# Optimization experiments

Measured on AMD Instinct MI355X. Metric: run time of the kernel, lower is better.

## Reference

```python
import jax, jax.numpy as jnp
import numpy as np

HEADS = 8
DIM_HEAD = 64
QUERY_DIM = 512
INNER = HEADS * DIM_HEAD
T = 16
MAX_REL = 16  # == temporal_length
SCALE = DIM_HEAD ** -0.5


def _rel_idx(length_q, length_k):
    rq = jnp.arange(length_q)
    rk = jnp.arange(length_k)
    dist = rk[None, :] - rq[:, None]
    return jnp.clip(dist, -MAX_REL, MAX_REL) + MAX_REL  # [Tq, Tk] in [0, 2*MAX_REL]


def setup_inputs() -> dict:
    key = jax.random.key(0)
    ks = jax.random.split(key, 8)
    B = 2048
    s = 0.02
    return {
        "x": jax.random.normal(ks[0], (B, T, QUERY_DIM), dtype=jnp.float32),
        "Wq": jax.random.normal(ks[1], (QUERY_DIM, INNER), dtype=jnp.float32) * s,
        "Wk": jax.random.normal(ks[2], (QUERY_DIM, INNER), dtype=jnp.float32) * s,
        "Wv": jax.random.normal(ks[3], (QUERY_DIM, INNER), dtype=jnp.float32) * s,
        "Wo": jax.random.normal(ks[4], (INNER, QUERY_DIM), dtype=jnp.float32) * s,
        "bo": jnp.zeros((QUERY_DIM,), dtype=jnp.float32),
        "rel_k_table": jax.random.normal(ks[5], (2 * MAX_REL + 1, DIM_HEAD), dtype=jnp.float32) * s,
        "rel_v_table": jax.random.normal(ks[6], (2 * MAX_REL + 1, DIM_HEAD), dtype=jnp.float32) * s,
    }


def reference(x, Wq, Wk, Wv, Wo, bo, rel_k_table, rel_v_table):
    B, N, _ = x.shape
    # projections (Linear without bias)
    def split_heads(t):
        return t.reshape(B, N, HEADS, DIM_HEAD).transpose(0, 2, 1, 3)  # [B, H, N, D]
    q = split_heads(x @ Wq)
    k = split_heads(x @ Wk)
    v = split_heads(x @ Wv)

    sim = jnp.einsum('bhid,bhjd->bhij', q, k) * SCALE
    idx = _rel_idx(N, N)                     # [N, N]
    k2 = rel_k_table[idx]                    # [N, N, D]
    sim = sim + jnp.einsum('bhtd,tsd->bhts', q, k2) * SCALE

    attn = jax.nn.softmax(sim, axis=-1)
    out = jnp.einsum('bhij,bhjd->bhid', attn, v)
    v2 = rel_v_table[idx]                    # [N, N, D]
    out = out + jnp.einsum('bhts,tsd->bhtd', attn, v2)

    out = out.transpose(0, 2, 1, 3).reshape(B, N, INNER)
    return out @ Wo + bo
```

## Files before the change

### kernel.cpp

```cpp
#include <hip/hip_runtime.h>
#include <stdint.h>


using bf16x8 = __attribute__((ext_vector_type(8))) short;
using f32x4  = __attribute__((ext_vector_type(4))) float;

#define AS3P(p) ((__attribute__((address_space(3))) void*)(p))
#define AS1P(p) ((const __attribute__((address_space(1))) void*)(p))

__device__ __forceinline__ uint16_t f2bf(float f) {
  unsigned int x = __builtin_bit_cast(unsigned int, f);
  x += 0x7fffu + ((x >> 16) & 1u);
  return (uint16_t)(x >> 16);
}

__global__ void cast_kernel(const float* __restrict__ in, uint16_t* __restrict__ out, int n8) {
  int i = blockIdx.x * 256 + threadIdx.x;
  if (i >= n8) return;
  float4 a = ((const float4*)in)[i * 2];
  float4 b = ((const float4*)in)[i * 2 + 1];
  uint4 r;
  r.x = (uint32_t)f2bf(a.x) | ((uint32_t)f2bf(a.y) << 16);
  r.y = (uint32_t)f2bf(a.z) | ((uint32_t)f2bf(a.w) << 16);
  r.z = (uint32_t)f2bf(b.x) | ((uint32_t)f2bf(b.y) << 16);
  r.w = (uint32_t)f2bf(b.z) | ((uint32_t)f2bf(b.w) << 16);
  ((uint4*)out)[i] = r;
}

__global__ void transpose_cast4(const float* __restrict__ Wq, const float* __restrict__ Wk,
                                const float* __restrict__ Wv, const float* __restrict__ Wo,
                                uint16_t* __restrict__ WqkvT, uint16_t* __restrict__ WoT) {
  __shared__ float tile[32][33];
  const int z = blockIdx.z;
  const float* src = (z == 0) ? Wq : (z == 1) ? Wk : (z == 2) ? Wv : Wo;
  uint16_t* dst = (z == 3) ? WoT : (WqkvT + z * 262144);
  int tx = threadIdx.x, ty = threadIdx.y;
  int c0 = blockIdx.x * 32, r0 = blockIdx.y * 32;
  #pragma unroll
  for (int k = 0; k < 4; ++k)
    tile[ty + 8 * k][tx] = src[(r0 + ty + 8 * k) * 512 + c0 + tx];
  __syncthreads();
  #pragma unroll
  for (int k = 0; k < 4; ++k)
    dst[(c0 + ty + 8 * k) * 512 + r0 + tx] = f2bf(tile[tx][ty + 8 * k]);
}

template<int OUT_MODE, int KDIM>
__global__ __launch_bounds__(256, 2) void gemm256(
    const uint16_t* __restrict__ A, const uint16_t* __restrict__ B,
    void* __restrict__ C, const float* __restrict__ bias, int N, int nbx) {
  constexpr int NT = KDIM / 32;
  __shared__ __align__(16) uint16_t ldsA[3][8192];
  __shared__ __align__(16) uint16_t ldsB[3][4096];
  __shared__ __align__(16) uint16_t ldsO[4][1024];
  const int tid = threadIdx.x;
  const int w = tid >> 6, l = tid & 63;
  const int lr = l & 15, kc = l >> 4;
  const int wm = w >> 1, wn = w & 1;
  const int cpx = gridDim.x >> 3;
  const int id = blockIdx.x;
  const int swz = (id & 7) * cpx + (id >> 3);
  const int by = swz / nbx, bx = swz - by * nbx;
  const int mBase = by * 256, nBase = bx * 128;
  const int g8 = l >> 3;
  const int sub = (l & 7) ^ g8;
  const uint16_t* gA = A + (size_t)(mBase + w * 64 + g8 * 2 + (sub >> 2)) * KDIM + (sub & 3) * 8;
  const uint16_t* gB = B + (size_t)(nBase + w * 32 + g8 * 2 + (sub >> 2)) * KDIM + (sub & 3) * 8;
  int offA[8], offB[4];
  #pragma unroll
  for (int m = 0; m < 8; ++m) {
    int row = wm * 128 + m * 16 + lr;
    int rp = row >> 1, sb = ((row & 1) << 2) | kc;
    offA[m] = rp * 128 + ((sb ^ (rp & 7)) << 4);
  }
  #pragma unroll
  for (int n = 0; n < 4; ++n) {
    int row = wn * 64 + n * 16 + lr;
    int rp = row >> 1, sb = ((row & 1) << 2) | kc;
    offB[n] = rp * 128 + ((sb ^ (rp & 7)) << 4);
  }
  f32x4 acc[8][4] = {};

#define STAGE_A(t, bf) do { \
    uint16_t* d = &ldsA[bf][w * 2048]; \
    const uint16_t* s = gA + (t) * 32; \
    __builtin_amdgcn_global_load_lds(AS1P(s),              AS3P(d),        16, 0, 0); \
    __builtin_amdgcn_global_load_lds(AS1P(s + 16 * KDIM),  AS3P(d + 512),  16, 0, 0); \
    __builtin_amdgcn_global_load_lds(AS1P(s + 32 * KDIM),  AS3P(d + 1024), 16, 0, 0); \
    __builtin_amdgcn_global_load_lds(AS1P(s + 48 * KDIM),  AS3P(d + 1536), 16, 0, 0); \
  } while (0)
#define STAGE_B(t, bf) do { \
    uint16_t* d = &ldsB[bf][w * 1024]; \
    const uint16_t* s = gB + (t) * 32; \
    __builtin_amdgcn_global_load_lds(AS1P(s),              AS3P(d),        16, 0, 0); \
    __builtin_amdgcn_global_load_lds(AS1P(s + 16 * KDIM),  AS3P(d + 512),  16, 0, 0); \
  } while (0)

  STAGE_A(0, 0); STAGE_B(0, 0);
  STAGE_A(1, 1); STAGE_B(1, 1);
  asm volatile("s_waitcnt vmcnt(6)" ::: "memory");
  __builtin_amdgcn_s_barrier();

  #pragma unroll
  for (int t = 0; t < NT; ++t) {
    const int bi = t % 3;
    const int si = (t + 2) % 3;
    const char* bufA = (const char*)&ldsA[bi][0];
    const char* bufB = (const char*)&ldsB[bi][0];
    if (t + 2 < NT) STAGE_A(t + 2, si);
    if (t + 2 < NT) asm volatile("s_waitcnt vmcnt(4)" ::: "memory");
    else            asm volatile("s_waitcnt vmcnt(0)" ::: "memory");
    bf16x8 a0 = *(const bf16x8*)(bufA + offA[0]);
    bf16x8 a1 = *(const bf16x8*)(bufA + offA[1]);
    bf16x8 a2 = *(const bf16x8*)(bufA + offA[2]);
    bf16x8 a3 = *(const bf16x8*)(bufA + offA[3]);
    bf16x8 b0 = *(const bf16x8*)(bufB + offB[0]);
    bf16x8 b1 = *(const bf16x8*)(bufB + offB[1]);
    bf16x8 b2 = *(const bf16x8*)(bufB + offB[2]);
    bf16x8 b3 = *(const bf16x8*)(bufB + offB[3]);
    __builtin_amdgcn_sched_barrier(0);
    __builtin_amdgcn_s_barrier();
    asm volatile("s_waitcnt lgkmcnt(0)" ::: "memory");
    __builtin_amdgcn_sched_barrier(0);
    __builtin_amdgcn_s_setprio(1);
    acc[0][0] = __builtin_amdgcn_mfma_f32_16x16x32_bf16(a0, b0, acc[0][0], 0, 0, 0);
    acc[0][1] = __builtin_amdgcn_mfma_f32_16x16x32_bf16(a0, b1, acc[0][1], 0, 0, 0);
    acc[0][2] = __builtin_amdgcn_mfma_f32_16x16x32_bf16(a0, b2, acc[0][2], 0, 0, 0);
    acc[0][3] = __builtin_amdgcn_mfma_f32_16x16x32_bf16(a0, b3, acc[0][3], 0, 0, 0);
    acc[1][0] = __builtin_amdgcn_mfma_f32_16x16x32_bf16(a1, b0, acc[1][0], 0, 0, 0);
    acc[1][1] = __builtin_amdgcn_mfma_f32_16x16x32_bf16(a1, b1, acc[1][1], 0, 0, 0);
    acc[1][2] = __builtin_amdgcn_mfma_f32_16x16x32_bf16(a1, b2, acc[1][2], 0, 0, 0);
    acc[1][3] = __builtin_amdgcn_mfma_f32_16x16x32_bf16(a1, b3, acc[1][3], 0, 0, 0);
    acc[2][0] = __builtin_amdgcn_mfma_f32_16x16x32_bf16(a2, b0, acc[2][0], 0, 0, 0);
    acc[2][1] = __builtin_amdgcn_mfma_f32_16x16x32_bf16(a2, b1, acc[2][1], 0, 0, 0);
    acc[2][2] = __builtin_amdgcn_mfma_f32_16x16x32_bf16(a2, b2, acc[2][2], 0, 0, 0);
    acc[2][3] = __builtin_amdgcn_mfma_f32_16x16x32_bf16(a2, b3, acc[2][3], 0, 0, 0);
    acc[3][0] = __builtin_amdgcn_mfma_f32_16x16x32_bf16(a3, b0, acc[3][0], 0, 0, 0);
    acc[3][1] = __builtin_amdgcn_mfma_f32_16x16x32_bf16(a3, b1, acc[3][1], 0, 0, 0);
    acc[3][2] = __builtin_amdgcn_mfma_f32_16x16x32_bf16(a3, b2, acc[3][2], 0, 0, 0);
    acc[3][3] = __builtin_amdgcn_mfma_f32_16x16x32_bf16(a3, b3, acc[3][3], 0, 0, 0);
    __builtin_amdgcn_s_setprio(0);
    __builtin_amdgcn_sched_barrier(0);
    __builtin_amdgcn_s_barrier();
    if (t + 2 < NT) STAGE_B(t + 2, si);
    bf16x8 a4 = *(const bf16x8*)(bufA + offA[4]);
    bf16x8 a5 = *(const bf16x8*)(bufA + offA[5]);
    bf16x8 a6 = *(const bf16x8*)(bufA + offA[6]);
    bf16x8 a7 = *(const bf16x8*)(bufA + offA[7]);
    __builtin_amdgcn_sched_barrier(0);
    __builtin_amdgcn_s_barrier();
    asm volatile("s_waitcnt lgkmcnt(0)" ::: "memory");
    __builtin_amdgcn_sched_barrier(0);
    __builtin_amdgcn_s_setprio(1);
    acc[4][0] = __builtin_amdgcn_mfma_f32_16x16x32_bf16(a4, b0, acc[4][0], 0, 0, 0);
    acc[4][1] = __builtin_amdgcn_mfma_f32_16x16x32_bf16(a4, b1, acc[4][1], 0, 0, 0);
    acc[4][2] = __builtin_amdgcn_mfma_f32_16x16x32_bf16(a4, b2, acc[4][2], 0, 0, 0);
    acc[4][3] = __builtin_amdgcn_mfma_f32_16x16x32_bf16(a4, b3, acc[4][3], 0, 0, 0);
    acc[5][0] = __builtin_amdgcn_mfma_f32_16x16x32_bf16(a5, b0, acc[5][0], 0, 0, 0);
    acc[5][1] = __builtin_amdgcn_mfma_f32_16x16x32_bf16(a5, b1, acc[5][1], 0, 0, 0);
    acc[5][2] = __builtin_amdgcn_mfma_f32_16x16x32_bf16(a5, b2, acc[5][2], 0, 0, 0);
    acc[5][3] = __builtin_amdgcn_mfma_f32_16x16x32_bf16(a5, b3, acc[5][3], 0, 0, 0);
    acc[6][0] = __builtin_amdgcn_mfma_f32_16x16x32_bf16(a6, b0, acc[6][0], 0, 0, 0);
    acc[6][1] = __builtin_amdgcn_mfma_f32_16x16x32_bf16(a6, b1, acc[6][1], 0, 0, 0);
    acc[6][2] = __builtin_amdgcn_mfma_f32_16x16x32_bf16(a6, b2, acc[6][2], 0, 0, 0);
    acc[6][3] = __builtin_amdgcn_mfma_f32_16x16x32_bf16(a6, b3, acc[6][3], 0, 0, 0);
    acc[7][0] = __builtin_amdgcn_mfma_f32_16x16x32_bf16(a7, b0, acc[7][0], 0, 0, 0);
    acc[7][1] = __builtin_amdgcn_mfma_f32_16x16x32_bf16(a7, b1, acc[7][1], 0, 0, 0);
    acc[7][2] = __builtin_amdgcn_mfma_f32_16x16x32_bf16(a7, b2, acc[7][2], 0, 0, 0);
    acc[7][3] = __builtin_amdgcn_mfma_f32_16x16x32_bf16(a7, b3, acc[7][3], 0, 0, 0);
    __builtin_amdgcn_s_setprio(0);
    __builtin_amdgcn_sched_barrier(0);
    __builtin_amdgcn_s_barrier();
  }
#undef STAGE_A
#undef STAGE_B
  if (OUT_MODE == 1) {
    uint16_t* oW = &ldsO[w][0];
    const int t2 = l >> 3, c2 = l & 7;
    const int grp = bx * 2 + wn;
    const int z = grp >> 3, h = grp & 7;
    uint16_t* gO = (uint16_t*)C + (size_t)h * 6291456 +
                   (size_t)(mBase + wm * 128 + t2) * 192 + z * 64 + c2 * 8;
    #pragma unroll
    for (int m = 0; m < 8; ++m) {
      #pragma unroll
      for (int n = 0; n < 4; ++n)
        #pragma unroll
        for (int r = 0; r < 4; ++r) {
          const int tt = kc * 4 + r;
          const int d = n * 16 + lr;
          const int col = (((d >> 3) ^ (tt & 7)) << 3) | (d & 7);
          oW[tt * 64 + col] = f2bf(acc[m][n][r]);
        }
      asm volatile("s_waitcnt lgkmcnt(0)" ::: "memory");
      __builtin_amdgcn_sched_barrier(0);
      bf16x8 s0 = *(const bf16x8*)(oW + t2 * 64 + (((c2 ^ (t2 & 7)) << 3)));
      bf16x8 s1 = *(const bf16x8*)(oW + (8 + t2) * 64 + (((c2 ^ (t2 & 7)) << 3)));
      *(bf16x8*)(gO + (size_t)(m * 16) * 192) = s0;
      *(bf16x8*)(gO + (size_t)(m * 16 + 8) * 192) = s1;
      asm volatile("s_waitcnt lgkmcnt(0)" ::: "memory");
      __builtin_amdgcn_sched_barrier(0);
    }
  } else {
    #pragma unroll
    for (int m = 0; m < 8; ++m)
      #pragma unroll
      for (int n = 0; n < 4; ++n) {
        const int col = nBase + wn * 64 + n * 16 + lr;
        #pragma unroll
        for (int r = 0; r < 4; ++r) {
          const int row = mBase + wm * 128 + m * 16 + kc * 4 + r;
          ((float*)C)[(size_t)row * N + col] = acc[m][n][r] + bias[col];
        }
      }
  }
}

__global__ __launch_bounds__(512) void attn_kernel(
    const uint16_t* __restrict__ qkv,
    const float* __restrict__ relk, const float* __restrict__ relv,
    uint16_t* __restrict__ outA) {
  __shared__ __align__(16) uint16_t relkS[33 * 72];
  __shared__ __align__(16) uint16_t relvT[64 * 40];
  __shared__ __align__(16) uint16_t vT[8][64 * 24];
  __shared__ float attnS[8][16 * 17];
  const int tid = threadIdx.x;
  for (int e = tid; e < 33 * 64; e += 512) {
    int j = e >> 6, d = e & 63;
    relkS[j * 72 + d] = f2bf(relk[e]);
    relvT[d * 40 + j] = f2bf(relv[e]);
  }
  const int w = tid >> 6, l = tid & 63;
  const int bh = blockIdx.x * 8 + w;
  const int b = bh >> 3, h = bh & 7;
  const int lr = l & 15, kc = l >> 4;
  const uint16_t* base = qkv + (size_t)h * 6291456 + (size_t)(b * 16) * 192;
  const uint16_t* qrow = base + lr * 192;
  bf16x8 aq0 = *(const bf16x8*)(qrow + kc * 8);
  bf16x8 aq1 = *(const bf16x8*)(qrow + 32 + kc * 8);
  const uint16_t* krow = qrow + 64;
  bf16x8 bk0 = *(const bf16x8*)(krow + kc * 8);
  bf16x8 bk1 = *(const bf16x8*)(krow + 32 + kc * 8);
  {
    const int s = l >> 2, dg = l & 3;
    const uint16_t* vrow = base + s * 192 + 128 + dg * 16;
    uint4 v0 = *(const uint4*)vrow;
    uint4 v1 = *(const uint4*)(vrow + 8);
    uint16_t tmp[16];
    *(uint4*)(tmp) = v0; *(uint4*)(tmp + 8) = v1;
    #pragma unroll
    for (int i = 0; i < 16; ++i)
      vT[w][(dg * 16 + i) * 24 + s] = tmp[i];
  }
  __syncthreads();
  const f32x4 zero = {0.f, 0.f, 0.f, 0.f};
  f32x4 sim = __builtin_amdgcn_mfma_f32_16x16x32_bf16(aq0, bk0, zero, 0, 0, 0);
  sim = __builtin_amdgcn_mfma_f32_16x16x32_bf16(aq1, bk1, sim, 0, 0, 0);
  bf16x8 rka0 = *(const bf16x8*)(relkS + lr * 72 + kc * 8);
  bf16x8 rka1 = *(const bf16x8*)(relkS + lr * 72 + 32 + kc * 8);
  bf16x8 rkb0 = *(const bf16x8*)(relkS + (16 + lr) * 72 + kc * 8);
  bf16x8 rkb1 = *(const bf16x8*)(relkS + (16 + lr) * 72 + 32 + kc * 8);
  f32x4 rqa = __builtin_amdgcn_mfma_f32_16x16x32_bf16(aq0, rka0, zero, 0, 0, 0);
  rqa = __builtin_amdgcn_mfma_f32_16x16x32_bf16(aq1, rka1, rqa, 0, 0, 0);
  f32x4 rqb = __builtin_amdgcn_mfma_f32_16x16x32_bf16(aq0, rkb0, zero, 0, 0, 0);
  rqb = __builtin_amdgcn_mfma_f32_16x16x32_bf16(aq1, rkb1, rqb, 0, 0, 0);
  #pragma unroll
  for (int r = 0; r < 4; ++r) {
    const int t = kc * 4 + r;
    const int j = lr - t + 16;
    const int src = (l & 48) | (j & 15);
    const float va = __shfl(rqa[r], src, 64);
    const float vb = __shfl(rqb[r], src, 64);
    const float rqv = (j < 16) ? va : vb;
    float sv = (sim[r] + rqv) * 0.125f;
    float m = sv;
    m = fmaxf(m, __shfl_xor(m, 1, 64));
    m = fmaxf(m, __shfl_xor(m, 2, 64));
    m = fmaxf(m, __shfl_xor(m, 4, 64));
    m = fmaxf(m, __shfl_xor(m, 8, 64));
    const float p = __expf(sv - m);
    float su = p;
    su += __shfl_xor(su, 1, 64);
    su += __shfl_xor(su, 2, 64);
    su += __shfl_xor(su, 4, 64);
    su += __shfl_xor(su, 8, 64);
    attnS[w][t * 17 + lr] = p / su;
  }
  __syncthreads();
  const float* aS = attnS[w];
  bf16x8 attnA, w2A;
  #pragma unroll
  for (int i = 0; i < 8; ++i) {
    const int s1 = kc * 8 + i;
    attnA[i] = (s1 < 16) ? (short)f2bf(aS[lr * 17 + s1]) : (short)0;
    const int s2 = s1 + lr - 16;
    w2A[i] = (s2 >= 0 && s2 < 16) ? (short)f2bf(aS[lr * 17 + s2]) : (short)0;
  }
  f32x4 o[4];
  #pragma unroll
  for (int dt = 0; dt < 4; ++dt) {
    bf16x8 vf  = *(const bf16x8*)(&vT[w][(dt * 16 + lr) * 24 + (kc & 1) * 8]);
    bf16x8 rvf = *(const bf16x8*)(&relvT[(dt * 16 + lr) * 40 + kc * 8]);
    o[dt] = __builtin_amdgcn_mfma_f32_16x16x32_bf16(w2A, rvf, zero, 0, 0, 0);
    o[dt] = __builtin_amdgcn_mfma_f32_16x16x32_bf16(attnA, vf, o[dt], 0, 0, 0);
  }
  asm volatile("s_waitcnt lgkmcnt(0)" ::: "memory");
  __builtin_amdgcn_sched_barrier(0);
  uint16_t* oW = &vT[w][0];
  #pragma unroll
  for (int dt = 0; dt < 4; ++dt)
    #pragma unroll
    for (int r = 0; r < 4; ++r) {
      const int t = kc * 4 + r;
      const int chunk = dt * 2 + (lr >> 3);
      oW[t * 64 + ((chunk ^ (t & 7)) << 3) + (lr & 7)] = f2bf(o[dt][r]);
    }
  asm volatile("s_waitcnt lgkmcnt(0)" ::: "memory");
  __builtin_amdgcn_sched_barrier(0);
  const int t2 = l >> 3, c2 = l & 7;
  bf16x8 s0 = *(const bf16x8*)(oW + t2 * 64 + ((c2 ^ (t2 & 7)) << 3));
  bf16x8 s1 = *(const bf16x8*)(oW + (8 + t2) * 64 + ((c2 ^ (t2 & 7)) << 3));
  *(bf16x8*)(outA + (size_t)(b * 16 + t2) * 512 + h * 64 + c2 * 8) = s0;
  *(bf16x8*)(outA + (size_t)(b * 16 + 8 + t2) * 512 + h * 64 + c2 * 8) = s1;
}

extern "C" void kernel_launch(void* const* d_in, const int* in_sizes, int n_in,
                              void* d_out, int out_size, void* d_ws, size_t ws_size,
                              hipStream_t stream) {
  const float* x    = (const float*)d_in[0];
  const float* Wq   = (const float*)d_in[1];
  const float* Wk   = (const float*)d_in[2];
  const float* Wv   = (const float*)d_in[3];
  const float* Wo   = (const float*)d_in[4];
  const float* bo   = (const float*)d_in[5];
  const float* relk = (const float*)d_in[6];
  const float* relv = (const float*)d_in[7];

  char* ws = (char*)d_ws;
  uint16_t* qkv   = (uint16_t*)ws;
  uint16_t* xbf   = (uint16_t*)(ws + 100663296);
  uint16_t* WqkvT = (uint16_t*)(ws + 134217728);
  uint16_t* WoT   = (uint16_t*)(ws + 135790592);
  uint16_t* attnO = xbf;

  cast_kernel<<<8192, 256, 0, stream>>>(x, xbf, 2097152);
  transpose_cast4<<<dim3(16, 16, 4), dim3(32, 8), 0, stream>>>(Wq, Wk, Wv, Wo, WqkvT, WoT);
  gemm256<1, 512><<<dim3(1536), dim3(256), 0, stream>>>(xbf, WqkvT, (void*)qkv, nullptr, 1536, 12);
  attn_kernel<<<2048, 512, 0, stream>>>(qkv, relk, relv, attnO);
  gemm256<0, 512><<<dim3(512), dim3(256), 0, stream>>>(attnO, WoT, d_out, bo, 512, 4);
}
```

Baseline: 140.2 us.

## Fuse fp32-to-bf16 cast of x into QKV GEMM A-tile staging

Removes the standalone cast kernel and has the QKV GEMM load fp32 activations into registers, convert them with packed bf16 conversion, and store them into swizzled LDS. The aim is to eliminate the round trip of writing and rereading a bf16 copy of x, plus one launch. In exchange, A is fetched in fp32 by every column block, and register staging replaces the async global-to-LDS loads, which raises VGPR use and changes the pipeline waits.

```diff
diff --git a/kernel.cpp b/kernel.cpp
--- a/kernel.cpp
+++ b/kernel.cpp
@@ -13,18 +13,10 @@
   x += 0x7fffu + ((x >> 16) & 1u);
   return (uint16_t)(x >> 16);
 }
-
-__global__ void cast_kernel(const float* __restrict__ in, uint16_t* __restrict__ out, int n8) {
-  int i = blockIdx.x * 256 + threadIdx.x;
-  if (i >= n8) return;
-  float4 a = ((const float4*)in)[i * 2];
-  float4 b = ((const float4*)in)[i * 2 + 1];
-  uint4 r;
-  r.x = (uint32_t)f2bf(a.x) | ((uint32_t)f2bf(a.y) << 16);
-  r.y = (uint32_t)f2bf(a.z) | ((uint32_t)f2bf(a.w) << 16);
-  r.z = (uint32_t)f2bf(b.x) | ((uint32_t)f2bf(b.y) << 16);
-  r.w = (uint32_t)f2bf(b.z) | ((uint32_t)f2bf(b.w) << 16);
-  ((uint4*)out)[i] = r;
+__device__ __forceinline__ uint32_t cvtpk(float lo, float hi) {
+  uint32_t r;
+  asm("v_cvt_pk_bf16_f32 %0, %1, %2" : "=v"(r) : "v"(lo), "v"(hi));
+  return r;
 }
 
 __global__ void transpose_cast4(const float* __restrict__ Wq, const float* __restrict__ Wk,
@@ -45,10 +37,10 @@
     dst[(c0 + ty + 8 * k) * 512 + r0 + tx] = f2bf(tile[tx][ty + 8 * k]);
 }
 
-template<int OUT_MODE, int KDIM>
-__global__ __launch_bounds__(256, 2) void gemm256(
-    const uint16_t* __restrict__ A, const uint16_t* __restrict__ B,
-    void* __restrict__ C, const float* __restrict__ bias, int N, int nbx) {
+template<int KDIM>
+__global__ __launch_bounds__(256, 2) void gemm1_f32a(
+    const float* __restrict__ A, const uint16_t* __restrict__ B,
+    uint16_t* __restrict__ C, int nbx) {
   constexpr int NT = KDIM / 32;
   __shared__ __align__(16) uint16_t ldsA[3][8192];
   __shared__ __align__(16) uint16_t ldsB[3][4096];
@@ -62,9 +54,17 @@
   const int swz = (id & 7) * cpx + (id >> 3);
   const int by = swz / nbx, bx = swz - by * nbx;
   const int mBase = by * 256, nBase = bx * 128;
+  const int ar = l >> 2, ac = l & 3;
+  const float* gA = A + (size_t)(mBase + w * 64 + ar) * KDIM + ac * 8;
+  int wofA[4];
+  #pragma unroll
+  for (int i = 0; i < 4; ++i) {
+    int row = w * 64 + i * 16 + ar;
+    int rp = row >> 1, sb = ((row & 1) << 2) | ac;
+    wofA[i] = rp * 128 + ((sb ^ (rp & 7)) << 4);
+  }
   const int g8 = l >> 3;
   const int sub = (l & 7) ^ g8;
-  const uint16_t* gA = A + (size_t)(mBase + w * 64 + g8 * 2 + (sub >> 2)) * KDIM + (sub & 3) * 8;
   const uint16_t* gB = B + (size_t)(nBase + w * 32 + g8 * 2 + (sub >> 2)) * KDIM + (sub & 3) * 8;
   int offA[8], offB[4];
   #pragma unroll
@@ -80,14 +80,27 @@
     offB[n] = rp * 128 + ((sb ^ (rp & 7)) << 4);
   }
   f32x4 acc[8][4] = {};
-
-#define STAGE_A(t, bf) do { \
-    uint16_t* d = &ldsA[bf][w * 2048]; \
-    const uint16_t* s = gA + (t) * 32; \
-    __builtin_amdgcn_global_load_lds(AS1P(s),              AS3P(d),        16, 0, 0); \
-    __builtin_amdgcn_global_load_lds(AS1P(s + 16 * KDIM),  AS3P(d + 512),  16, 0, 0); \
-    __builtin_amdgcn_global_load_lds(AS1P(s + 32 * KDIM),  AS3P(d + 1024), 16, 0, 0); \
-    __builtin_amdgcn_global_load_lds(AS1P(s + 48 * KDIM),  AS3P(d + 1536), 16, 0, 0); \
+  f32x4 ra[2][8];
+
+#define LOAD_A(t, rb) do { \
+    const float* s = gA + (t) * 32; \
+    _Pragma("unroll") \
+    for (int i = 0; i < 4; ++i) { \
+      ra[rb][2 * i]     = *(const f32x4*)(s + i * 16 * KDIM); \
+      ra[rb][2 * i + 1] = *(const f32x4*)(s + i * 16 * KDIM + 4); \
+    } \
+  } while (0)
+#define WRITE_A(bf, rb) do { \
+    uint16_t* d = &ldsA[bf][0]; \
+    _Pragma("unroll") \
+    for (int i = 0; i < 4; ++i) { \
+      int4 q; \
+      q.x = (int)cvtpk(ra[rb][2 * i][0], ra[rb][2 * i][1]); \
+      q.y = (int)cvtpk(ra[rb][2 * i][2], ra[rb][2 * i][3]); \
+      q.z = (int)cvtpk(ra[rb][2 * i + 1][0], ra[rb][2 * i + 1][1]); \
+      q.w = (int)cvtpk(ra[rb][2 * i + 1][2], ra[rb][2 * i + 1][3]); \
+      *(int4*)((char*)d + wofA[i]) = q; \
+    } \
   } while (0)
 #define STAGE_B(t, bf) do { \
     uint16_t* d = &ldsB[bf][w * 1024]; \
@@ -96,20 +109,23 @@
     __builtin_amdgcn_global_load_lds(AS1P(s + 16 * KDIM),  AS3P(d + 512),  16, 0, 0); \
   } while (0)
 
-  STAGE_A(0, 0); STAGE_B(0, 0);
-  STAGE_A(1, 1); STAGE_B(1, 1);
-  asm volatile("s_waitcnt vmcnt(6)" ::: "memory");
+  LOAD_A(0, 0);
+  asm volatile("s_waitcnt vmcnt(0)" ::: "memory");
+  WRITE_A(0, 0);
+  STAGE_B(0, 0);
+  LOAD_A(1, 1);
+  STAGE_B(1, 1);
+  asm volatile("s_waitcnt vmcnt(10)" ::: "memory");
+  asm volatile("s_waitcnt lgkmcnt(0)" ::: "memory");
+  __builtin_amdgcn_sched_barrier(0);
   __builtin_amdgcn_s_barrier();
 
   #pragma unroll
   for (int t = 0; t < NT; ++t) {
     const int bi = t % 3;
-    const int si = (t + 2) % 3;
     const char* bufA = (const char*)&ldsA[bi][0];
     const char* bufB = (const char*)&ldsB[bi][0];
-    if (t + 2 < NT) STAGE_A(t + 2, si);
-    if (t + 2 < NT) asm volatile("s_waitcnt vmcnt(4)" ::: "memory");
-    else            asm volatile("s_waitcnt vmcnt(0)" ::: "memory");
+    if (t + 2 < NT) LOAD_A(t + 2, t & 1);
     bf16x8 a0 = *(const bf16x8*)(bufA + offA[0]);
     bf16x8 a1 = *(const bf16x8*)(bufA + offA[1]);
     bf16x8 a2 = *(const bf16x8*)(bufA + offA[2]);
@@ -142,11 +158,15 @@
     __builtin_amdgcn_s_setprio(0);
     __builtin_amdgcn_sched_barrier(0);
     __builtin_amdgcn_s_barrier();
-    if (t + 2 < NT) STAGE_B(t + 2, si);
+    if (t + 2 < NT) STAGE_B(t + 2, (t + 2) % 3);
     bf16x8 a4 = *(const bf16x8*)(bufA + offA[4]);
     bf16x8 a5 = *(const bf16x8*)(bufA + offA[5]);
     bf16x8 a6 = *(const bf16x8*)(bufA + offA[6]);
     bf16x8 a7 = *(const bf16x8*)(bufA + offA[7]);
+    if (t + 2 < NT)      asm volatile("s_waitcnt vmcnt(10)" ::: "memory");
+    else if (t + 1 < NT) asm volatile("s_waitcnt vmcnt(0)" ::: "memory");
+    __builtin_amdgcn_sched_barrier(0);
+    if (t + 1 < NT) WRITE_A((t + 1) % 3, (t + 1) & 1);
     __builtin_amdgcn_sched_barrier(0);
     __builtin_amdgcn_s_barrier();
     asm volatile("s_waitcnt lgkmcnt(0)" ::: "memory");
@@ -172,14 +192,15 @@
     __builtin_amdgcn_sched_barrier(0);
     __builtin_amdgcn_s_barrier();
   }
-#undef STAGE_A
+#undef LOAD_A
+#undef WRITE_A
 #undef STAGE_B
-  if (OUT_MODE == 1) {
+  {
     uint16_t* oW = &ldsO[w][0];
     const int t2 = l >> 3, c2 = l & 7;
     const int grp = bx * 2 + wn;
     const int z = grp >> 3, h = grp & 7;
-    uint16_t* gO = (uint16_t*)C + (size_t)h * 6291456 +
+    uint16_t* gO = C + (size_t)h * 6291456 +
                    (size_t)(mBase + wm * 128 + t2) * 192 + z * 64 + c2 * 8;
     #pragma unroll
     for (int m = 0; m < 8; ++m) {
@@ -201,19 +222,145 @@
       asm volatile("s_waitcnt lgkmcnt(0)" ::: "memory");
       __builtin_amdgcn_sched_barrier(0);
     }
-  } else {
+  }
+}
+
+template<int KDIM>
+__global__ __launch_bounds__(256, 2) void gemm256(
+    const uint16_t* __restrict__ A, const uint16_t* __restrict__ B,
+    float* __restrict__ C, const float* __restrict__ bias, int N, int nbx) {
+  constexpr int NT = KDIM / 32;
+  __shared__ __align__(16) uint16_t ldsA[3][8192];
+  __shared__ __align__(16) uint16_t ldsB[3][4096];
+  const int tid = threadIdx.x;
+  const int w = tid >> 6, l = tid & 63;
+  const int lr = l & 15, kc = l >> 4;
+  const int wm = w >> 1, wn = w & 1;
+  const int cpx = gridDim.x >> 3;
+  const int id = blockIdx.x;
+  const int swz = (id & 7) * cpx + (id >> 3);
+  const int by = swz / nbx, bx = swz - by * nbx;
+  const int mBase = by * 256, nBase = bx * 128;
+  const int g8 = l >> 3;
+  const int sub = (l & 7) ^ g8;
+  const uint16_t* gA = A + (size_t)(mBase + w * 64 + g8 * 2 + (sub >> 2)) * KDIM + (sub & 3) * 8;
+  const uint16_t* gB = B + (size_t)(nBase + w * 32 + g8 * 2 + (sub >> 2)) * KDIM + (sub & 3) * 8;
+  int offA[8], offB[4];
+  #pragma unroll
+  for (int m = 0; m < 8; ++m) {
+    int row = wm * 128 + m * 16 + lr;
+    int rp = row >> 1, sb = ((row & 1) << 2) | kc;
+    offA[m] = rp * 128 + ((sb ^ (rp & 7)) << 4);
+  }
+  #pragma unroll
+  for (int n = 0; n < 4; ++n) {
+    int row = wn * 64 + n * 16 + lr;
+    int rp = row >> 1, sb = ((row & 1) << 2) | kc;
+    offB[n] = rp * 128 + ((sb ^ (rp & 7)) << 4);
+  }
+  f32x4 acc[8][4] = {};
+#define STAGE_A(t, bf) do { \
+    uint16_t* d = &ldsA[bf][w * 2048]; \
+    const uint16_t* s = gA + (t) * 32; \
+    __builtin_amdgcn_global_load_lds(AS1P(s),              AS3P(d),        16, 0, 0); \
+    __builtin_amdgcn_global_load_lds(AS1P(s + 16 * KDIM),  AS3P(d + 512),  16, 0, 0); \
+    __builtin_amdgcn_global_load_lds(AS1P(s + 32 * KDIM),  AS3P(d + 1024), 16, 0, 0); \
+    __builtin_amdgcn_global_load_lds(AS1P(s + 48 * KDIM),  AS3P(d + 1536), 16, 0, 0); \
+  } while (0)
+#define STAGE_B(t, bf) do { \
+    uint16_t* d = &ldsB[bf][w * 1024]; \
+    const uint16_t* s = gB + (t) * 32; \
+    __builtin_amdgcn_global_load_lds(AS1P(s),              AS3P(d),        16, 0, 0); \
+    __builtin_amdgcn_global_load_lds(AS1P(s + 16 * KDIM),  AS3P(d + 512),  16, 0, 0); \
+  } while (0)
+  STAGE_A(0, 0); STAGE_B(0, 0);
+  STAGE_A(1, 1); STAGE_B(1, 1);
+  asm volatile("s_waitcnt vmcnt(6)" ::: "memory");
+  __builtin_amdgcn_s_barrier();
+  #pragma unroll
+  for (int t = 0; t < NT; ++t) {
+    const int bi = t % 3;
+    const int si = (t + 2) % 3;
+    const char* bufA = (const char*)&ldsA[bi][0];
+    const char* bufB = (const char*)&ldsB[bi][0];
+    if (t + 2 < NT) STAGE_A(t + 2, si);
+    if (t + 2 < NT) asm volatile("s_waitcnt vmcnt(4)" ::: "memory");
+    else            asm volatile("s_waitcnt vmcnt(0)" ::: "memory");
+    bf16x8 a0 = *(const bf16x8*)(bufA + offA[0]);
+    bf16x8 a1 = *(const bf16x8*)(bufA + offA[1]);
+    bf16x8 a2 = *(const bf16x8*)(bufA + offA[2]);
+    bf16x8 a3 = *(const bf16x8*)(bufA + offA[3]);
+    bf16x8 b0 = *(const bf16x8*)(bufB + offB[0]);
+    bf16x8 b1 = *(const bf16x8*)(bufB + offB[1]);
+    bf16x8 b2 = *(const bf16x8*)(bufB + offB[2]);
+    bf16x8 b3 = *(const bf16x8*)(bufB + offB[3]);
+    __builtin_amdgcn_sched_barrier(0);
+    __builtin_amdgcn_s_barrier();
+    asm volatile("s_waitcnt lgkmcnt(0)" ::: "memory");
+    __builtin_amdgcn_sched_barrier(0);
+    __builtin_amdgcn_s_setprio(1);
+    acc[0][0] = __builtin_amdgcn_mfma_f32_16x16x32_bf16(a0, b0, acc[0][0], 0, 0, 0);
+    acc[0][1] = __builtin_amdgcn_mfma_f32_16x16x32_bf16(a0, b1, acc[0][1], 0, 0, 0);
+    acc[0][2] = __builtin_amdgcn_mfma_f32_16x16x32_bf16(a0, b2, acc[0][2], 0, 0, 0);
+    acc[0][3] = __builtin_amdgcn_mfma_f32_16x16x32_bf16(a0, b3, acc[0][3], 0, 0, 0);
+    acc[1][0] = __builtin_amdgcn_mfma_f32_16x16x32_bf16(a1, b0, acc[1][0], 0, 0, 0);
+    acc[1][1] = __builtin_amdgcn_mfma_f32_16x16x32_bf16(a1, b1, acc[1][1], 0, 0, 0);
+    acc[1][2] = __builtin_amdgcn_mfma_f32_16x16x32_bf16(a1, b2, acc[1][2], 0, 0, 0);
+    acc[1][3] = __builtin_amdgcn_mfma_f32_16x16x32_bf16(a1, b3, acc[1][3], 0, 0, 0);
+    acc[2][0] = __builtin_amdgcn_mfma_f32_16x16x32_bf16(a2, b0, acc[2][0], 0, 0, 0);
+    acc[2][1] = __builtin_amdgcn_mfma_f32_16x16x32_bf16(a2, b1, acc[2][1], 0, 0, 0);
+    acc[2][2] = __builtin_amdgcn_mfma_f32_16x16x32_bf16(a2, b2, acc[2][2], 0, 0, 0);
+    acc[2][3] = __builtin_amdgcn_mfma_f32_16x16x32_bf16(a2, b3, acc[2][3], 0, 0, 0);
+    acc[3][0] = __builtin_amdgcn_mfma_f32_16x16x32_bf16(a3, b0, acc[3][0], 0, 0, 0);
+    acc[3][1] = __builtin_amdgcn_mfma_f32_16x16x32_bf16(a3, b1, acc[3][1], 0, 0, 0);
+    acc[3][2] = __builtin_amdgcn_mfma_f32_16x16x32_bf16(a3, b2, acc[3][2], 0, 0, 0);
+    acc[3][3] = __builtin_amdgcn_mfma_f32_16x16x32_bf16(a3, b3, acc[3][3], 0, 0, 0);
+    __builtin_amdgcn_s_setprio(0);
+    __builtin_amdgcn_sched_barrier(0);
+    __builtin_amdgcn_s_barrier();
+    if (t + 2 < NT) STAGE_B(t + 2, si);
+    bf16x8 a4 = *(const bf16x8*)(bufA + offA[4]);
+    bf16x8 a5 = *(const bf16x8*)(bufA + offA[5]);
+    bf16x8 a6 = *(const bf16x8*)(bufA + offA[6]);
+    bf16x8 a7 = *(const bf16x8*)(bufA + offA[7]);
+    __builtin_amdgcn_sched_barrier(0);
+    __builtin_amdgcn_s_barrier();
+    asm volatile("s_waitcnt lgkmcnt(0)" ::: "memory");
+    __builtin_amdgcn_sched_barrier(0);
+    __builtin_amdgcn_s_setprio(1);
+    acc[4][0] = __builtin_amdgcn_mfma_f32_16x16x32_bf16(a4, b0, acc[4][0], 0, 0, 0);
+    acc[4][1] = __builtin_amdgcn_mfma_f32_16x16x32_bf16(a4, b1, acc[4][1], 0, 0, 0);
+    acc[4][2] = __builtin_amdgcn_mfma_f32_16x16x32_bf16(a4, b2, acc[4][2], 0, 0, 0);
+    acc[4][3] = __builtin_amdgcn_mfma_f32_16x16x32_bf16(a4, b3, acc[4][3], 0, 0, 0);
+    acc[5][0] = __builtin_amdgcn_mfma_f32_16x16x32_bf16(a5, b0, acc[5][0], 0, 0, 0);
+    acc[5][1] = __builtin_amdgcn_mfma_f32_16x16x32_bf16(a5, b1, acc[5][1], 0, 0, 0);
+    acc[5][2] = __builtin_amdgcn_mfma_f32_16x16x32_bf16(a5, b2, acc[5][2], 0, 0, 0);
+    acc[5][3] = __builtin_amdgcn_mfma_f32_16x16x32_bf16(a5, b3, acc[5][3], 0, 0, 0);
+    acc[6][0] = __builtin_amdgcn_mfma_f32_16x16x32_bf16(a6, b0, acc[6][0], 0, 0, 0);
+    acc[6][1] = __builtin_amdgcn_mfma_f32_16x16x32_bf16(a6, b1, acc[6][1], 0, 0, 0);
+    acc[6][2] = __builtin_amdgcn_mfma_f32_16x16x32_bf16(a6, b2, acc[6][2], 0, 0, 0);
+    acc[6][3] = __builtin_amdgcn_mfma_f32_16x16x32_bf16(a6, b3, acc[6][3], 0, 0, 0);
+    acc[7][0] = __builtin_amdgcn_mfma_f32_16x16x32_bf16(a7, b0, acc[7][0], 0, 0, 0);
+    acc[7][1] = __builtin_amdgcn_mfma_f32_16x16x32_bf16(a7, b1, acc[7][1], 0, 0, 0);
+    acc[7][2] = __builtin_amdgcn_mfma_f32_16x16x32_bf16(a7, b2, acc[7][2], 0, 0, 0);
+    acc[7][3] = __builtin_amdgcn_mfma_f32_16x16x32_bf16(a7, b3, acc[7][3], 0, 0, 0);
+    __builtin_amdgcn_s_setprio(0);
+    __builtin_amdgcn_sched_barrier(0);
+    __builtin_amdgcn_s_barrier();
+  }
+#undef STAGE_A
+#undef STAGE_B
+  #pragma unroll
+  for (int m = 0; m < 8; ++m)
     #pragma unroll
-    for (int m = 0; m < 8; ++m)
+    for (int n = 0; n < 4; ++n) {
+      const int col = nBase + wn * 64 + n * 16 + lr;
       #pragma unroll
-      for (int n = 0; n < 4; ++n) {
-        const int col = nBase + wn * 64 + n * 16 + lr;
-        #pragma unroll
-        for (int r = 0; r < 4; ++r) {
-          const int row = mBase + wm * 128 + m * 16 + kc * 4 + r;
-          ((float*)C)[(size_t)row * N + col] = acc[m][n][r] + bias[col];
-        }
+      for (int r = 0; r < 4; ++r) {
+        const int row = mBase + wm * 128 + m * 16 + kc * 4 + r;
+        C[(size_t)row * N + col] = acc[m][n][r] + bias[col];
       }
-  }
+    }
 }
 
 __global__ __launch_bounds__(512) void attn_kernel(
@@ -338,14 +485,12 @@
 
   char* ws = (char*)d_ws;
   uint16_t* qkv   = (uint16_t*)ws;
-  uint16_t* xbf   = (uint16_t*)(ws + 100663296);
+  uint16_t* attnO = (uint16_t*)(ws + 100663296);
   uint16_t* WqkvT = (uint16_t*)(ws + 134217728);
   uint16_t* WoT   = (uint16_t*)(ws + 135790592);
-  uint16_t* attnO = xbf;
-
-  cast_kernel<<<8192, 256, 0, stream>>>(x, xbf, 2097152);
+
   transpose_cast4<<<dim3(16, 16, 4), dim3(32, 8), 0, stream>>>(Wq, Wk, Wv, Wo, WqkvT, WoT);
-  gemm256<1, 512><<<dim3(1536), dim3(256), 0, stream>>>(xbf, WqkvT, (void*)qkv, nullptr, 1536, 12);
+  gemm1_f32a<512><<<dim3(1536), dim3(256), 0, stream>>>(x, WqkvT, qkv, 12);
   attn_kernel<<<2048, 512, 0, stream>>>(qkv, relk, relv, attnO);
-  gemm256<0, 512><<<dim3(512), dim3(256), 0, stream>>>(attnO, WoT, d_out, bo, 512, 4);
-}
+  gemm256<512><<<dim3(512), dim3(256), 0, stream>>>(attnO, WoT, (float*)d_out, bo, 512, 4);
+}
```

Measured after the change: 151.3 us. 7.9% more time.
